# Kernel optimization log

Hardware: AMD Instinct MI355X
Metric: run time of the kernel (lower is better)

## Reference

```python
import jax, jax.numpy as jnp
import numpy as np

B, T, S, C, H = 2, 2048, 2048, 1024, 16
D = C // H  # head dim = 64


def setup_inputs() -> dict:
    key = jax.random.key(0)
    ks = jax.random.split(key, 6)
    sc = 1.0 / np.sqrt(C)
    return {
        "q": jax.random.normal(ks[0], (B, T, C), jnp.float32),
        "p": jax.random.normal(ks[1], (B, S, C), jnp.float32),
        "Wq": jax.random.normal(ks[2], (C, C), jnp.float32) * sc,
        "Wk": jax.random.normal(ks[3], (C, C), jnp.float32) * sc,
        "Wv": jax.random.normal(ks[4], (C, C), jnp.float32) * sc,
        "Wo": jax.random.normal(ks[5], (C, C), jnp.float32) * sc,
    }


def reference(q, p, Wq, Wk, Wv, Wo):
    # Linear projections (no bias: config.bias=True -> nn.Linear bias=False)
    qh = (q @ Wq).reshape(B, T, H, D)  # [B,T,H,D]
    kh = (p @ Wk).reshape(B, S, H, D)  # [B,S,H,D]
    vh = (p @ Wv).reshape(B, S, H, D)  # [B,S,H,D]
    scale = 1.0 / jnp.sqrt(jnp.asarray(D, qh.dtype))
    att = jnp.einsum('bthd,bshd->bhts', qh, kh) * scale  # [B,H,T,S]
    att = jax.nn.softmax(att, axis=-1)
    y = jnp.einsum('bhts,bshd->bthd', att, vh).reshape(B, T, C)
    y = y @ Wo  # c_proj, dropout p=0 (eval)
    return y
```

## Files before the change

kernel.cpp:

```cpp
#include <hip/hip_runtime.h>
#include <hip/hip_bf16.h>
#include <stdint.h>

#define T_LEN 2048
#define CDIM  1024

typedef short bf16x8_t  __attribute__((ext_vector_type(8)));
typedef float f32x4_t   __attribute__((ext_vector_type(4)));
typedef float f32x16_t  __attribute__((ext_vector_type(16)));

__device__ __forceinline__ float fexp2(float x) {
  float r;
  asm("v_exp_f32 %0, %1" : "=v"(r) : "v"(x));
  return r;
}

__device__ __forceinline__ void gload_lds16(const void* gptr, void* lptr) {
  __builtin_amdgcn_global_load_lds(
      (const __attribute__((address_space(1))) unsigned int*)(gptr),
      (__attribute__((address_space(3))) unsigned int*)(lptr),
      16, 0, 0);
}

__device__ __forceinline__ unsigned short f2bf(float f) {
  union { float f; unsigned int u; } v; v.f = f;
  unsigned int u = v.u;
  return (unsigned short)((u + 0x7fffu + ((u >> 16) & 1u)) >> 16);
}

__device__ __forceinline__ unsigned int pk_bf16(float lo, float hi) {
  unsigned int r;
  asm("v_cvt_pk_bf16_f32 %0, %1, %2" : "=v"(r) : "v"(lo), "v"(hi));
  return r;
}
__device__ __forceinline__ unsigned short bf1(float v) {
  return (unsigned short)pk_bf16(v, v);
}

__global__ __launch_bounds__(256) void cast2_f32_bf16(const float* __restrict__ x0,
                                                      const float* __restrict__ x1,
                                                      unsigned short* __restrict__ y0,
                                                      unsigned short* __restrict__ y1) {
  int i = blockIdx.x * 256 + threadIdx.x;
  const float* x = blockIdx.y ? x1 : x0;
  unsigned short* y = blockIdx.y ? y1 : y0;
  const float4* x4 = (const float4*)x;
  float4 a = x4[i * 2], b = x4[i * 2 + 1];
  union { unsigned short u[8]; uint4 v; } o;
  o.u[0] = f2bf(a.x); o.u[1] = f2bf(a.y); o.u[2] = f2bf(a.z); o.u[3] = f2bf(a.w);
  o.u[4] = f2bf(b.x); o.u[5] = f2bf(b.y); o.u[6] = f2bf(b.z); o.u[7] = f2bf(b.w);
  ((uint4*)y)[i] = o.v;
}

__global__ __launch_bounds__(256) void transpose_cast4(const float* __restrict__ W0,
                                                       const float* __restrict__ W1,
                                                       const float* __restrict__ W2,
                                                       const float* __restrict__ W3,
                                                       unsigned short* __restrict__ Wall,
                                                       unsigned short* __restrict__ Wot) {
  __shared__ float tile[32][33];
  int z = blockIdx.z;
  const float* W = (z == 0) ? W0 : (z == 1) ? W1 : (z == 2) ? W2 : W3;
  unsigned short* Wt = (z < 3) ? (Wall + (size_t)z * 1024 * 1024) : Wot;
  int tx = threadIdx.x & 31, ty = threadIdx.x >> 5;
  int n0 = blockIdx.x * 32, k0 = blockIdx.y * 32;
#pragma unroll
  for (int i = 0; i < 4; ++i) {
    int r = ty + i * 8;
    tile[r][tx] = W[(size_t)(k0 + r) * CDIM + n0 + tx];
  }
  __syncthreads();
#pragma unroll
  for (int i = 0; i < 4; ++i) {
    int r = ty + i * 8;
    Wt[(size_t)(n0 + r) * CDIM + k0 + tx] = f2bf(tile[tx][r]);
  }
}

__global__ __launch_bounds__(256) void gemm_qkv(const unsigned short* __restrict__ qbm,
                                                const unsigned short* __restrict__ pbm,
                                                const unsigned short* __restrict__ Wall,
                                                unsigned short* __restrict__ Qh,
                                                unsigned short* __restrict__ Kh,
                                                unsigned short* __restrict__ Vt) {
  __shared__ unsigned short ldsA[128 * 64];
  __shared__ unsigned short ldsB[64 * 64];
  const int tid = threadIdx.x, lane = tid & 63, w = tid >> 6;
  const int bid = blockIdx.x;
  const int xcd = bid & 7, local = bid >> 3;
  const int pm = xcd & 3, pn = xcd >> 2;
  const int lm = local & 7, ln = local >> 3;
  const int mblk = pm * 8 + lm;
  const int nblk = pn * 24 + ln;
  const int m0 = mblk * 128;
  const int n0 = nblk * 64;
  const char* Ab = (const char*)((nblk < 16) ? qbm : pbm);
  const char* Bb = (const char*)Wall;
  char* lA = (char*)ldsA;
  char* lB = (char*)ldsB;
  f32x4_t acc[2][4] = {};

  for (int kt = 0; kt < 16; ++kt) {
#pragma unroll
    for (int it = 0; it < 4; ++it) {
      int ob = it * 4096 + w * 1024;
      int o = ob + lane * 16;
      int row = o >> 7, cin = o & 127;
      int cs = cin ^ ((row & 7) << 4);
      gload_lds16(Ab + (size_t)(m0 + row) * 2048 + kt * 128 + cs, lA + ob);
    }
#pragma unroll
    for (int it = 0; it < 2; ++it) {
      int ob = it * 4096 + w * 1024;
      int o = ob + lane * 16;
      int row = o >> 7, cin = o & 127;
      int cs = cin ^ ((row & 7) << 4);
      gload_lds16(Bb + (size_t)(n0 + row) * 2048 + kt * 128 + cs, lB + ob);
    }
    __syncthreads();
#pragma unroll
    for (int kf = 0; kf < 2; ++kf) {
      int c = kf * 64 + ((lane >> 4) << 4);
      bf16x8_t af[2], bfr[4];
#pragma unroll
      for (int mf = 0; mf < 2; ++mf) {
        int row = w * 32 + mf * 16 + (lane & 15);
        af[mf] = *(const bf16x8_t*)(lA + row * 128 + (c ^ ((row & 7) << 4)));
      }
#pragma unroll
      for (int nf = 0; nf < 4; ++nf) {
        int row = nf * 16 + (lane & 15);
        bfr[nf] = *(const bf16x8_t*)(lB + row * 128 + (c ^ ((row & 7) << 4)));
      }
#pragma unroll
      for (int mf = 0; mf < 2; ++mf)
#pragma unroll
        for (int nf = 0; nf < 4; ++nf)
          acc[mf][nf] = __builtin_amdgcn_mfma_f32_16x16x32_bf16(af[mf], bfr[nf], acc[mf][nf], 0, 0, 0);
    }
    __syncthreads();
  }

  const float oscale = (nblk < 16) ? 0.18033688011112042f : 1.0f;
#pragma unroll
  for (int mf = 0; mf < 2; ++mf)
#pragma unroll
    for (int nf = 0; nf < 4; ++nf)
#pragma unroll
      for (int j = 0; j < 4; ++j) {
        int row = m0 + w * 32 + mf * 16 + ((lane >> 4) << 2) + j;
        int col = n0 + nf * 16 + (lane & 15);
        float v = acc[mf][nf][j] * oscale;
        int b = row >> 11, ts = row & 2047;
        if (col < 1024) {
          int h = col >> 6, d = col & 63;
          Qh[(((size_t)(b * 16 + h)) * 2048 + ts) * 64 + d] = bf1(v);
        } else if (col < 2048) {
          int cc = col - 1024, h = cc >> 6, d = cc & 63;
          Kh[(((size_t)(b * 16 + h)) * 2048 + ts) * 64 + d] = bf1(v);
        } else {
          int cc = col - 2048, h = cc >> 6, d = cc & 63;
          Vt[(((size_t)(b * 16 + h)) * 64 + d) * 2048 + ts] = bf1(v);
        }
      }
}

__global__ __launch_bounds__(256) void gemm_out(const unsigned short* __restrict__ A,
                                                const unsigned short* __restrict__ Bt,
                                                float* __restrict__ Out) {
  __shared__ unsigned short ldsA[128 * 64];
  __shared__ unsigned short ldsB[64 * 64];
  const int tid = threadIdx.x, lane = tid & 63, w = tid >> 6;
  const int bid = blockIdx.x;
  const int xcd = bid & 7, local = bid >> 3;
  const int pm = xcd & 3, pn = xcd >> 2;
  const int lm = local & 7, ln = local >> 3;
  const int m0 = (pm * 8 + lm) * 128;
  const int n0 = (pn * 8 + ln) * 64;
  const char* Ab = (const char*)A;
  const char* Bb = (const char*)Bt;
  char* lA = (char*)ldsA;
  char* lB = (char*)ldsB;
  f32x4_t acc[2][4] = {};

  for (int kt = 0; kt < 16; ++kt) {
#pragma unroll
    for (int it = 0; it < 4; ++it) {
      int ob = it * 4096 + w * 1024;
      int o = ob + lane * 16;
      int row = o >> 7, cin = o & 127;
      int cs = cin ^ ((row & 7) << 4);
      gload_lds16(Ab + (size_t)(m0 + row) * 2048 + kt * 128 + cs, lA + ob);
    }
#pragma unroll
    for (int it = 0; it < 2; ++it) {
      int ob = it * 4096 + w * 1024;
      int o = ob + lane * 16;
      int row = o >> 7, cin = o & 127;
      int cs = cin ^ ((row & 7) << 4);
      gload_lds16(Bb + (size_t)(n0 + row) * 2048 + kt * 128 + cs, lB + ob);
    }
    __syncthreads();
#pragma unroll
    for (int kf = 0; kf < 2; ++kf) {
      int c = kf * 64 + ((lane >> 4) << 4);
      bf16x8_t af[2], bfr[4];
#pragma unroll
      for (int mf = 0; mf < 2; ++mf) {
        int row = w * 32 + mf * 16 + (lane & 15);
        af[mf] = *(const bf16x8_t*)(lA + row * 128 + (c ^ ((row & 7) << 4)));
      }
#pragma unroll
      for (int nf = 0; nf < 4; ++nf) {
        int row = nf * 16 + (lane & 15);
        bfr[nf] = *(const bf16x8_t*)(lB + row * 128 + (c ^ ((row & 7) << 4)));
      }
#pragma unroll
      for (int mf = 0; mf < 2; ++mf)
#pragma unroll
        for (int nf = 0; nf < 4; ++nf)
          acc[mf][nf] = __builtin_amdgcn_mfma_f32_16x16x32_bf16(af[mf], bfr[nf], acc[mf][nf], 0, 0, 0);
    }
    __syncthreads();
  }

#pragma unroll
  for (int mf = 0; mf < 2; ++mf)
#pragma unroll
    for (int nf = 0; nf < 4; ++nf)
#pragma unroll
      for (int j = 0; j < 4; ++j) {
        int row = m0 + w * 32 + mf * 16 + ((lane >> 4) << 2) + j;
        int col = n0 + nf * 16 + (lane & 15);
        Out[(size_t)row * 1024 + col] = acc[mf][nf][j];
      }
}

template <int SPLIT>
__global__ __launch_bounds__(256, 3) void attn32(const unsigned short* __restrict__ Qg,
                                                 const unsigned short* __restrict__ Kg,
                                                 const unsigned short* __restrict__ Vtg,
                                                 unsigned short* __restrict__ Ag,
                                                 float* __restrict__ OpA,
                                                 float* __restrict__ OpB,
                                                 float* __restrict__ Lp) {
  __shared__ unsigned short ldsK[3][64 * 64];
  __shared__ unsigned short ldsV[2][64 * 64];
  const int tid = threadIdx.x, lane = tid & 63, w = tid >> 6;
  const int hi = lane >> 5, ql = lane & 31;
  const int bid = blockIdx.x;
  int bh, z, qtile;
  if (SPLIT == 2) {
    int comb = bid & 63;
    qtile = bid >> 6;
    bh = comb >> 1;
    z = comb & 1;
  } else {
    bh = bid & 31;
    qtile = bid >> 5;
    z = 0;
  }
  const int q0 = qtile * 128 + w * 32;
  constexpr int NT = 2048 / SPLIT / 64;
  const int sBeg = z * (2048 / SPLIT);

  bf16x8_t qf[4];
#pragma unroll
  for (int kd = 0; kd < 4; ++kd)
    qf[kd] = *(const bf16x8_t*)(Qg + ((size_t)bh * T_LEN + q0 + ql) * 64 + kd * 16 + hi * 8);

  bf16x8_t ones;
#pragma unroll
  for (int i = 0; i < 8; ++i) ones[i] = (short)0x3F80;

  f32x16_t oacc[2] = {};
  f32x16_t lacc = {};
  const f32x16_t vzero = {};

  const char* Kb = (const char*)(Kg + (size_t)bh * 2048 * 64);
  const char* Vb = (const char*)(Vtg + (size_t)bh * 64 * 2048);

  auto stageK = [&](int slot, int t) {
    int s0 = sBeg + t * 64;
#pragma unroll
    for (int it = 0; it < 2; ++it) {
      int ob = it * 4096 + w * 1024;
      int o = ob + lane * 16;
      int row = o >> 7, cin = o & 127;
      int cs = cin ^ ((row & 7) << 4);
      gload_lds16(Kb + (size_t)s0 * 128 + row * 128 + cs, (char*)ldsK[slot] + ob);
    }
  };
  auto stageV = [&](int slot, int t) {
    int s0 = sBeg + t * 64;
#pragma unroll
    for (int it = 0; it < 2; ++it) {
      int ob = it * 4096 + w * 1024;
      int o = ob + lane * 16;
      int row = o >> 7, cin = o & 127;
      int cs = cin ^ ((row & 7) << 4);
      gload_lds16(Vb + (size_t)s0 * 2 + (size_t)row * 4096 + cs, (char*)ldsV[slot] + ob);
    }
  };

  auto qk = [&](f32x16_t (&s)[2], int slot) {
    const char* lK = (const char*)ldsK[slot];
#pragma unroll
    for (int sub = 0; sub < 2; ++sub) {
      int row = sub * 32 + ql;
      int swz = (row & 7) << 4;
#pragma unroll
      for (int kd = 0; kd < 4; ++kd) {
        bf16x8_t kfrag = *(const bf16x8_t*)(lK + row * 128 + ((kd * 32 + hi * 16) ^ swz));
        s[sub] = __builtin_amdgcn_mfma_f32_32x32x16_bf16(kfrag, qf[kd], s[sub], 0, 0, 0);
      }
    }
  };

  auto consume = [&](f32x16_t (&s)[2], int vslot) {
    const char* lV = (const char*)ldsV[vslot];
#pragma unroll
    for (int ks = 0; ks < 4; ++ks) {
      const int sub = ks >> 1, mA = (ks & 1) * 2, mB = mA + 1;
      float e0 = fexp2(s[sub][4 * mA + 0]), e1 = fexp2(s[sub][4 * mA + 1]);
      float e2 = fexp2(s[sub][4 * mA + 2]), e3 = fexp2(s[sub][4 * mA + 3]);
      float e4 = fexp2(s[sub][4 * mB + 0]), e5 = fexp2(s[sub][4 * mB + 1]);
      float e6 = fexp2(s[sub][4 * mB + 2]), e7 = fexp2(s[sub][4 * mB + 3]);
      unsigned int a0 = pk_bf16(e0, e1), a1 = pk_bf16(e2, e3);
      unsigned int b0 = pk_bf16(e4, e5), b1 = pk_bf16(e6, e7);
      asm("v_permlane32_swap_b32 %0, %1" : "+v"(a0), "+v"(b0));
      asm("v_permlane32_swap_b32 %0, %1" : "+v"(a1), "+v"(b1));
      union { unsigned int u[4]; bf16x8_t v; } P;
      P.u[0] = a0; P.u[1] = a1; P.u[2] = b0; P.u[3] = b1;
      lacc = __builtin_amdgcn_mfma_f32_32x32x16_bf16(P.v, ones, lacc, 0, 0, 0);
#pragma unroll
      for (int dt = 0; dt < 2; ++dt) {
        int row = dt * 32 + ql;
        bf16x8_t vfrag = *(const bf16x8_t*)(lV + row * 128 + ((ks * 32 + hi * 16) ^ ((row & 7) << 4)));
        oacc[dt] = __builtin_amdgcn_mfma_f32_32x32x16_bf16(P.v, vfrag, oacc[dt], 0, 0, 0);
      }
    }
  };

  f32x16_t sA[2] = {}, sB[2] = {};
  stageK(0, 0);
  stageV(0, 0);
  stageK(1, 1);
  __syncthreads();
  qk(sA, 0);

  for (int i = 0; i < NT; i += 2) {
    if (i + 2 < NT) stageK((i + 2) % 3, i + 2);
    if (i + 1 < NT) stageV((i + 1) & 1, i + 1);
    if (i + 1 < NT) { sB[0] = vzero; sB[1] = vzero; qk(sB, (i + 1) % 3); }
    consume(sA, i & 1);
    __syncthreads();
    if (i + 1 < NT) {
      if (i + 3 < NT) stageK((i + 3) % 3, i + 3);
      if (i + 2 < NT) stageV((i + 2) & 1, i + 2);
      if (i + 2 < NT) { sA[0] = vzero; sA[1] = vzero; qk(sA, (i + 2) % 3); }
      consume(sB, (i + 1) & 1);
      __syncthreads();
    }
  }

  const int b = bh >> 4, h = bh & 15;
  if (SPLIT == 1) {
#pragma unroll
    for (int grp = 0; grp < 4; ++grp)
#pragma unroll
      for (int r2 = 0; r2 < 4; ++r2) {
        int reg = grp * 4 + r2;
        float linv = 1.0f / lacc[reg];
        int t = q0 + 4 * hi + 8 * grp + r2;
#pragma unroll
        for (int dt = 0; dt < 2; ++dt) {
          int col = h * 64 + dt * 32 + ql;
          float v = oacc[dt][reg] * linv;
          Ag[((size_t)b * T_LEN + t) * CDIM + col] = bf1(v);
        }
      }
  } else {
    float* Op = z ? OpB : OpA;
#pragma unroll
    for (int grp = 0; grp < 4; ++grp)
#pragma unroll
      for (int r2 = 0; r2 < 4; ++r2) {
        int reg = grp * 4 + r2;
        int t = q0 + 4 * hi + 8 * grp + r2;
#pragma unroll
        for (int dt = 0; dt < 2; ++dt)
          Op[((size_t)b * T_LEN + t) * CDIM + h * 64 + dt * 32 + ql] = oacc[dt][reg];
        if (ql == 0)
          Lp[(((size_t)z * 2 + b) * 16 + h) * T_LEN + t] = lacc[reg];
      }
  }
}

__global__ __launch_bounds__(256) void attn_combine(const float* __restrict__ O0,
                                                    const float* __restrict__ O1,
                                                    const float* __restrict__ Lp,
                                                    unsigned short* __restrict__ Ag) {
  int i = blockIdx.x * 256 + threadIdx.x;
  int c8 = i & 127, bt = i >> 7;
  int b = bt >> 11, t = bt & 2047;
  int c = c8 * 8, h = c >> 6;
  float l0 = Lp[(((size_t)0 * 2 + b) * 16 + h) * T_LEN + t];
  float l1 = Lp[(((size_t)1 * 2 + b) * 16 + h) * T_LEN + t];
  float inv = 1.0f / (l0 + l1);
  size_t off = (size_t)bt * CDIM + c;
  float4 x0 = *(const float4*)(O0 + off);
  float4 x1 = *(const float4*)(O1 + off);
  float4 y0 = *(const float4*)(O0 + off + 4);
  float4 y1 = *(const float4*)(O1 + off + 4);
  union { unsigned int u[4]; uint4 v; } o;
  o.u[0] = pk_bf16((x0.x + x1.x) * inv, (x0.y + x1.y) * inv);
  o.u[1] = pk_bf16((x0.z + x1.z) * inv, (x0.w + x1.w) * inv);
  o.u[2] = pk_bf16((y0.x + y1.x) * inv, (y0.y + y1.y) * inv);
  o.u[3] = pk_bf16((y0.z + y1.z) * inv, (y0.w + y1.w) * inv);
  *(uint4*)(Ag + off) = o.v;
}

extern "C" void kernel_launch(void* const* d_in, const int* in_sizes, int n_in,
                              void* d_out, int out_size, void* d_ws, size_t ws_size,
                              hipStream_t stream) {
  const float* q  = (const float*)d_in[0];
  const float* p  = (const float*)d_in[1];
  const float* Wq = (const float*)d_in[2];
  const float* Wk = (const float*)d_in[3];
  const float* Wv = (const float*)d_in[4];
  const float* Wo = (const float*)d_in[5];

  char* ws = (char*)d_ws;
  const size_t MB = (size_t)1 << 20;
  unsigned short* qb   = (unsigned short*)(ws);
  unsigned short* pb   = (unsigned short*)(ws + 8 * MB);
  unsigned short* Wall = (unsigned short*)(ws + 16 * MB);
  unsigned short* Wot  = (unsigned short*)(ws + 22 * MB);
  unsigned short* Qh   = (unsigned short*)(ws + 24 * MB);
  unsigned short* Kh   = (unsigned short*)(ws + 32 * MB);
  unsigned short* Vt   = (unsigned short*)(ws + 40 * MB);
  unsigned short* Ao   = (unsigned short*)(ws + 48 * MB);

  cast2_f32_bf16<<<dim3(2048, 2), 256, 0, stream>>>(q, p, qb, pb);
  transpose_cast4<<<dim3(32, 32, 4), 256, 0, stream>>>(Wq, Wk, Wv, Wo, Wall, Wot);

  gemm_qkv<<<1536, 256, 0, stream>>>(qb, pb, Wall, Qh, Kh, Vt);

  if (ws_size >= 73 * MB) {
    float* O0 = (float*)(ws);
    float* O1 = (float*)(ws + 56 * MB);
    float* Lp = (float*)(ws + 72 * MB);
    attn32<2><<<1024, 256, 0, stream>>>(Qh, Kh, Vt, nullptr, O0, O1, Lp);
    attn_combine<<<2048, 256, 0, stream>>>(O0, O1, Lp, Ao);
  } else {
    attn32<1><<<512, 256, 0, stream>>>(Qh, Kh, Vt, Ao, nullptr, nullptr, nullptr);
  }

  gemm_out<<<512, 256, 0, stream>>>(Ao, Wot, (float*)d_out);
}
```

Before: 132.8 us.

## Double-buffer GEMM LDS tiles and store split-attention partials in bf16

Both projection GEMMs now use two LDS buffers per operand and prefetch the tile two steps ahead, so global-to-LDS loads overlap the MFMA work. There is a single barrier per iteration instead of two. Separately, the split-KV attention partial outputs are written as bf16 instead of fp32, which halves their write and read traffic in the attention and combine kernels. The cost is twice the LDS per GEMM block, which may lower occupancy, and lower precision on the partial sums before they are combined.

```diff
diff --git a/kernel.cpp b/kernel.cpp
--- a/kernel.cpp
+++ b/kernel.cpp
@@ -22,6 +22,13 @@
       16, 0, 0);
 }
 
+__device__ __forceinline__ void wait_vm0_barrier() {
+  asm volatile("s_waitcnt vmcnt(0)" ::: "memory");
+  __builtin_amdgcn_sched_barrier(0);
+  __builtin_amdgcn_s_barrier();
+  __builtin_amdgcn_sched_barrier(0);
+}
+
 __device__ __forceinline__ unsigned short f2bf(float f) {
   union { float f; unsigned int u; } v; v.f = f;
   unsigned int u = v.u;
@@ -35,6 +42,10 @@
 }
 __device__ __forceinline__ unsigned short bf1(float v) {
   return (unsigned short)pk_bf16(v, v);
+}
+__device__ __forceinline__ float bf2f(unsigned short u) {
+  union { unsigned int u; float f; } v; v.u = ((unsigned int)u) << 16;
+  return v.f;
 }
 
 __global__ __launch_bounds__(256) void cast2_f32_bf16(const float* __restrict__ x0,
@@ -83,8 +94,8 @@
                                                 unsigned short* __restrict__ Qh,
                                                 unsigned short* __restrict__ Kh,
                                                 unsigned short* __restrict__ Vt) {
-  __shared__ unsigned short ldsA[128 * 64];
-  __shared__ unsigned short ldsB[64 * 64];
+  __shared__ unsigned short ldsA[2][128 * 64];
+  __shared__ unsigned short ldsB[2][64 * 64];
   const int tid = threadIdx.x, lane = tid & 63, w = tid >> 6;
   const int bid = blockIdx.x;
   const int xcd = bid & 7, local = bid >> 3;
@@ -96,28 +107,33 @@
   const int n0 = nblk * 64;
   const char* Ab = (const char*)((nblk < 16) ? qbm : pbm);
   const char* Bb = (const char*)Wall;
-  char* lA = (char*)ldsA;
-  char* lB = (char*)ldsB;
   f32x4_t acc[2][4] = {};
 
+  auto stage = [&](int buf, int kt) {
+#pragma unroll
+    for (int it = 0; it < 4; ++it) {
+      int ob = it * 4096 + w * 1024;
+      int o = ob + lane * 16;
+      int row = o >> 7, cin = o & 127;
+      int cs = cin ^ ((row & 7) << 4);
+      gload_lds16(Ab + (size_t)(m0 + row) * 2048 + kt * 128 + cs, (char*)ldsA[buf] + ob);
+    }
+#pragma unroll
+    for (int it = 0; it < 2; ++it) {
+      int ob = it * 4096 + w * 1024;
+      int o = ob + lane * 16;
+      int row = o >> 7, cin = o & 127;
+      int cs = cin ^ ((row & 7) << 4);
+      gload_lds16(Bb + (size_t)(n0 + row) * 2048 + kt * 128 + cs, (char*)ldsB[buf] + ob);
+    }
+  };
+
+  stage(0, 0);
+  wait_vm0_barrier();
+  stage(1, 1);
   for (int kt = 0; kt < 16; ++kt) {
-#pragma unroll
-    for (int it = 0; it < 4; ++it) {
-      int ob = it * 4096 + w * 1024;
-      int o = ob + lane * 16;
-      int row = o >> 7, cin = o & 127;
-      int cs = cin ^ ((row & 7) << 4);
-      gload_lds16(Ab + (size_t)(m0 + row) * 2048 + kt * 128 + cs, lA + ob);
-    }
-#pragma unroll
-    for (int it = 0; it < 2; ++it) {
-      int ob = it * 4096 + w * 1024;
-      int o = ob + lane * 16;
-      int row = o >> 7, cin = o & 127;
-      int cs = cin ^ ((row & 7) << 4);
-      gload_lds16(Bb + (size_t)(n0 + row) * 2048 + kt * 128 + cs, lB + ob);
-    }
-    __syncthreads();
+    const char* lA = (const char*)ldsA[kt & 1];
+    const char* lB = (const char*)ldsB[kt & 1];
 #pragma unroll
     for (int kf = 0; kf < 2; ++kf) {
       int c = kf * 64 + ((lane >> 4) << 4);
@@ -138,7 +154,10 @@
         for (int nf = 0; nf < 4; ++nf)
           acc[mf][nf] = __builtin_amdgcn_mfma_f32_16x16x32_bf16(af[mf], bfr[nf], acc[mf][nf], 0, 0, 0);
     }
-    __syncthreads();
+    if (kt < 15) {
+      wait_vm0_barrier();
+      if (kt + 2 < 16) stage(kt & 1, kt + 2);
+    }
   }
 
   const float oscale = (nblk < 16) ? 0.18033688011112042f : 1.0f;
@@ -168,8 +187,8 @@
 __global__ __launch_bounds__(256) void gemm_out(const unsigned short* __restrict__ A,
                                                 const unsigned short* __restrict__ Bt,
                                                 float* __restrict__ Out) {
-  __shared__ unsigned short ldsA[128 * 64];
-  __shared__ unsigned short ldsB[64 * 64];
+  __shared__ unsigned short ldsA[2][128 * 64];
+  __shared__ unsigned short ldsB[2][64 * 64];
   const int tid = threadIdx.x, lane = tid & 63, w = tid >> 6;
   const int bid = blockIdx.x;
   const int xcd = bid & 7, local = bid >> 3;
@@ -179,28 +198,33 @@
   const int n0 = (pn * 8 + ln) * 64;
   const char* Ab = (const char*)A;
   const char* Bb = (const char*)Bt;
-  char* lA = (char*)ldsA;
-  char* lB = (char*)ldsB;
   f32x4_t acc[2][4] = {};
 
+  auto stage = [&](int buf, int kt) {
+#pragma unroll
+    for (int it = 0; it < 4; ++it) {
+      int ob = it * 4096 + w * 1024;
+      int o = ob + lane * 16;
+      int row = o >> 7, cin = o & 127;
+      int cs = cin ^ ((row & 7) << 4);
+      gload_lds16(Ab + (size_t)(m0 + row) * 2048 + kt * 128 + cs, (char*)ldsA[buf] + ob);
+    }
+#pragma unroll
+    for (int it = 0; it < 2; ++it) {
+      int ob = it * 4096 + w * 1024;
+      int o = ob + lane * 16;
+      int row = o >> 7, cin = o & 127;
+      int cs = cin ^ ((row & 7) << 4);
+      gload_lds16(Bb + (size_t)(n0 + row) * 2048 + kt * 128 + cs, (char*)ldsB[buf] + ob);
+    }
+  };
+
+  stage(0, 0);
+  wait_vm0_barrier();
+  stage(1, 1);
   for (int kt = 0; kt < 16; ++kt) {
-#pragma unroll
-    for (int it = 0; it < 4; ++it) {
-      int ob = it * 4096 + w * 1024;
-      int o = ob + lane * 16;
-      int row = o >> 7, cin = o & 127;
-      int cs = cin ^ ((row & 7) << 4);
-      gload_lds16(Ab + (size_t)(m0 + row) * 2048 + kt * 128 + cs, lA + ob);
-    }
-#pragma unroll
-    for (int it = 0; it < 2; ++it) {
-      int ob = it * 4096 + w * 1024;
-      int o = ob + lane * 16;
-      int row = o >> 7, cin = o & 127;
-      int cs = cin ^ ((row & 7) << 4);
-      gload_lds16(Bb + (size_t)(n0 + row) * 2048 + kt * 128 + cs, lB + ob);
-    }
-    __syncthreads();
+    const char* lA = (const char*)ldsA[kt & 1];
+    const char* lB = (const char*)ldsB[kt & 1];
 #pragma unroll
     for (int kf = 0; kf < 2; ++kf) {
       int c = kf * 64 + ((lane >> 4) << 4);
@@ -221,7 +245,10 @@
         for (int nf = 0; nf < 4; ++nf)
           acc[mf][nf] = __builtin_amdgcn_mfma_f32_16x16x32_bf16(af[mf], bfr[nf], acc[mf][nf], 0, 0, 0);
     }
-    __syncthreads();
+    if (kt < 15) {
+      wait_vm0_barrier();
+      if (kt + 2 < 16) stage(kt & 1, kt + 2);
+    }
   }
 
 #pragma unroll
@@ -241,8 +268,8 @@
                                                  const unsigned short* __restrict__ Kg,
                                                  const unsigned short* __restrict__ Vtg,
                                                  unsigned short* __restrict__ Ag,
-                                                 float* __restrict__ OpA,
-                                                 float* __restrict__ OpB,
+                                                 unsigned short* __restrict__ OpA,
+                                                 unsigned short* __restrict__ OpB,
                                                  float* __restrict__ Lp) {
   __shared__ unsigned short ldsK[3][64 * 64];
   __shared__ unsigned short ldsV[2][64 * 64];
@@ -381,7 +408,7 @@
         }
       }
   } else {
-    float* Op = z ? OpB : OpA;
+    unsigned short* Op = z ? OpB : OpA;
 #pragma unroll
     for (int grp = 0; grp < 4; ++grp)
 #pragma unroll
@@ -390,15 +417,15 @@
         int t = q0 + 4 * hi + 8 * grp + r2;
 #pragma unroll
         for (int dt = 0; dt < 2; ++dt)
-          Op[((size_t)b * T_LEN + t) * CDIM + h * 64 + dt * 32 + ql] = oacc[dt][reg];
+          Op[((size_t)b * T_LEN + t) * CDIM + h * 64 + dt * 32 + ql] = bf1(oacc[dt][reg]);
         if (ql == 0)
           Lp[(((size_t)z * 2 + b) * 16 + h) * T_LEN + t] = lacc[reg];
       }
   }
 }
 
-__global__ __launch_bounds__(256) void attn_combine(const float* __restrict__ O0,
-                                                    const float* __restrict__ O1,
+__global__ __launch_bounds__(256) void attn_combine(const unsigned short* __restrict__ O0,
+                                                    const unsigned short* __restrict__ O1,
                                                     const float* __restrict__ Lp,
                                                     unsigned short* __restrict__ Ag) {
   int i = blockIdx.x * 256 + threadIdx.x;
@@ -409,15 +436,15 @@
   float l1 = Lp[(((size_t)1 * 2 + b) * 16 + h) * T_LEN + t];
   float inv = 1.0f / (l0 + l1);
   size_t off = (size_t)bt * CDIM + c;
-  float4 x0 = *(const float4*)(O0 + off);
-  float4 x1 = *(const float4*)(O1 + off);
-  float4 y0 = *(const float4*)(O0 + off + 4);
-  float4 y1 = *(const float4*)(O1 + off + 4);
-  union { unsigned int u[4]; uint4 v; } o;
-  o.u[0] = pk_bf16((x0.x + x1.x) * inv, (x0.y + x1.y) * inv);
-  o.u[1] = pk_bf16((x0.z + x1.z) * inv, (x0.w + x1.w) * inv);
-  o.u[2] = pk_bf16((y0.x + y1.x) * inv, (y0.y + y1.y) * inv);
-  o.u[3] = pk_bf16((y0.z + y1.z) * inv, (y0.w + y1.w) * inv);
+  union { unsigned short u[8]; uint4 v; } a, bb, o;
+  a.v  = *(const uint4*)(O0 + off);
+  bb.v = *(const uint4*)(O1 + off);
+  float s[8];
+#pragma unroll
+  for (int k = 0; k < 8; ++k) s[k] = (bf2f(a.u[k]) + bf2f(bb.u[k])) * inv;
+  unsigned int p0 = pk_bf16(s[0], s[1]), p1 = pk_bf16(s[2], s[3]);
+  unsigned int p2 = pk_bf16(s[4], s[5]), p3 = pk_bf16(s[6], s[7]);
+  o.v = make_uint4(p0, p1, p2, p3);
   *(uint4*)(Ag + off) = o.v;
 }
 
@@ -448,8 +475,8 @@
   gemm_qkv<<<1536, 256, 0, stream>>>(qb, pb, Wall, Qh, Kh, Vt);
 
   if (ws_size >= 73 * MB) {
-    float* O0 = (float*)(ws);
-    float* O1 = (float*)(ws + 56 * MB);
+    unsigned short* O0 = (unsigned short*)(ws);
+    unsigned short* O1 = (unsigned short*)(ws + 56 * MB);
     float* Lp = (float*)(ws + 72 * MB);
     attn32<2><<<1024, 256, 0, stream>>>(Qh, Kh, Vt, nullptr, O0, O1, Lp);
     attn_combine<<<2048, 256, 0, stream>>>(O0, O1, Lp, Ao);
```

Result: faster. 130.0 us, median of 2 (-2.0%).
